# Optimization experiments

Measured on AMD Instinct MI355X. Metric: run time of the kernel, lower is better.

Reference implementation:

```python
import jax, jax.numpy as jnp
import numpy as np


def setup_inputs() -> dict:
    key = jax.random.key(0)
    ks = jax.random.split(key, 6)
    B, L, D, E = 4, 2048, 1024, 4
    H = 4 * D
    x = jax.random.normal(ks[0], (B, L, D), dtype=jnp.float32)
    # router: Linear(D, 2D) -> GELU -> Linear(2D, E); kaiming-ish init
    rW1 = jax.random.normal(ks[1], (D, 2 * D), dtype=jnp.float32) * (2.0 / D) ** 0.5
    rb1 = jnp.zeros((2 * D,), dtype=jnp.float32)
    rW2 = jax.random.normal(ks[2], (2 * D, E), dtype=jnp.float32) * (2.0 / (2 * D)) ** 0.5
    rb2 = jnp.zeros((E,), dtype=jnp.float32)
    # experts: Linear(D, 4D) -> GELU -> Linear(4D, D), stacked over E
    We1 = jax.random.normal(ks[3], (E, D, H), dtype=jnp.float32) * (2.0 / D) ** 0.5
    be1 = jnp.zeros((E, H), dtype=jnp.float32)
    We2 = jax.random.normal(ks[4], (E, H, D), dtype=jnp.float32) * (2.0 / H) ** 0.5
    be2 = jnp.zeros((E, D), dtype=jnp.float32)
    return {"x": x, "rW1": rW1, "rb1": rb1, "rW2": rW2, "rb2": rb2,
            "We1": We1, "be1": be1, "We2": We2, "be2": be2}


def reference(x, rW1, rb1, rW2, rb2, We1, be1, We2, be2):
    E = We1.shape[0]
    top_k = min(2, E)
    # router (dropouts are identity in eval mode)
    rh = jax.nn.gelu(x @ rW1 + rb1, approximate=False)          # [B,L,2D]
    router_logits = rh @ rW2 + rb2                               # [B,L,E]
    router_probs = jax.nn.softmax(router_logits, axis=-1)
    expert_weights, expert_indices = jax.lax.top_k(router_probs, top_k)  # [B,L,k]
    one_hot = jax.nn.one_hot(expert_indices, E, dtype=x.dtype)   # [B,L,k,E]
    token_mask = one_hot.sum(axis=2)                             # [B,L,E] 1 if expert selected
    combine_w = (one_hot * expert_weights[..., None]).sum(axis=2)  # [B,L,E] gate weight per expert
    out = jnp.zeros_like(x)
    for e in range(E):  # fixed small expert count; dense per-expert MLP over all tokens (as original)
        xi = x * token_mask[..., e:e + 1]
        h = jax.nn.gelu(xi @ We1[e] + be1[e], approximate=False)  # [B,L,4D]
        yo = h @ We2[e] + be2[e]                                  # [B,L,D]
        out = out + yo * combine_w[..., e:e + 1]
    return out
```

## Files before the change

### kernel.cpp

```cpp
#include <hip/hip_runtime.h>
#include <math.h>


typedef short bf16x8 __attribute__((ext_vector_type(8)));
typedef float f32x4 __attribute__((ext_vector_type(4)));
typedef unsigned short u16;

__device__ __forceinline__ u16 f2bf(float f) {
  unsigned u = __float_as_uint(f);
  u += 0x7FFFu + ((u >> 16) & 1u);
  return (u16)(u >> 16);
}
__device__ __forceinline__ float bf2f(u16 s) {
  return __uint_as_float(((unsigned)s) << 16);
}
__device__ __forceinline__ float gelu_f(float x) {
  return 0.5f * x * (1.0f + erff(x * 0.70710678118654752f));
}
__device__ __forceinline__ float gelu_fast(float x) {
  float y = 1.5957691216057308f * (x + 0.044715f * x * x * x);
  float e = __expf(y);
  float t = 1.0f - 2.0f * __builtin_amdgcn_rcpf(e + 1.0f);
  return 0.5f * x * (1.0f + t);
}
__device__ __forceinline__ void gload_lds16(const void* g, void* l) {
  __builtin_amdgcn_global_load_lds(
      (const __attribute__((address_space(1))) void*)g,
      (__attribute__((address_space(3))) void*)l, 16, 0, 0);
}

__global__ __launch_bounds__(256) void convert_split_kernel(
    const float* __restrict__ in, u16* __restrict__ hi, u16* __restrict__ lo,
    int n4) {
  int i = blockIdx.x * blockDim.x + threadIdx.x;
  int stride = gridDim.x * blockDim.x;
  for (; i < n4; i += stride) {
    float4 v = ((const float4*)in)[i];
    float f[4] = {v.x, v.y, v.z, v.w};
    ushort4 h4, l4;
    u16* hp = (u16*)&h4;
    u16* lp = (u16*)&l4;
#pragma unroll
    for (int u = 0; u < 4; ++u) {
      u16 h = f2bf(f[u]);
      hp[u] = h;
      lp[u] = f2bf(f[u] - bf2f(h));
    }
    ((ushort4*)hi)[i] = h4;
    ((ushort4*)lo)[i] = l4;
  }
}

__global__ __launch_bounds__(256) void transpose_split_kernel(
    const float* __restrict__ in, u16* __restrict__ hi, u16* __restrict__ lo,
    int R, int C) {
  __shared__ float tile[32][33];
  const int c0 = blockIdx.x * 32, r0 = blockIdx.y * 32;
#pragma unroll
  for (int i = 0; i < 4; ++i) {
    int rr = threadIdx.y + i * 8;
    tile[rr][threadIdx.x] = in[(size_t)(r0 + rr) * C + c0 + threadIdx.x];
  }
  __syncthreads();
#pragma unroll
  for (int i = 0; i < 4; ++i) {
    int cc = threadIdx.y + i * 8;
    float v = tile[threadIdx.x][cc];
    u16 h = f2bf(v);
    size_t oidx = (size_t)(c0 + cc) * R + r0 + threadIdx.x;
    hi[oidx] = h;
    lo[oidx] = f2bf(v - bf2f(h));
  }
}

__global__ __launch_bounds__(256) void transpose_pair_kernel(
    const float* __restrict__ We1, const float* __restrict__ We2,
    u16* __restrict__ T1, u16* __restrict__ T2, size_t tstride, int e0) {
  __shared__ float tile[32][33];
  const int e = e0 + blockIdx.y;
  int b = blockIdx.x;
  const float* in;
  u16* out;
  int R, C, tx, ty;
  if (b < 4096) {
    in = We1 + (size_t)e * 1024 * 4096;
    out = T1 + (size_t)blockIdx.y * tstride;
    R = 1024; C = 4096; tx = b & 127; ty = b >> 7;
  } else {
    b -= 4096;
    in = We2 + (size_t)e * 1024 * 4096;
    out = T2 + (size_t)blockIdx.y * tstride;
    R = 4096; C = 1024; tx = b & 31; ty = b >> 5;
  }
  const int c0 = tx * 32, r0 = ty * 32;
#pragma unroll
  for (int i = 0; i < 4; ++i) {
    int rr = threadIdx.y + i * 8;
    tile[rr][threadIdx.x] = in[(size_t)(r0 + rr) * C + c0 + threadIdx.x];
  }
  __syncthreads();
#pragma unroll
  for (int i = 0; i < 4; ++i) {
    int cc = threadIdx.y + i * 8;
    out[(size_t)(c0 + cc) * R + r0 + threadIdx.x] = f2bf(tile[threadIdx.x][cc]);
  }
}

__global__ __launch_bounds__(256) void gemm3_router_kernel(
    const u16* __restrict__ Ahi, const u16* __restrict__ Alo,
    const u16* __restrict__ Bhi, const u16* __restrict__ Blo, int K,
    const float* __restrict__ bias, const float* __restrict__ rW2,
    float* __restrict__ parts) {
  __shared__ alignas(16) u16 Sm[4 * 128 * 32];
  __shared__ float pls[2][128][4];
  const int tid = threadIdx.x;
  const int lane = tid & 63;
  const int w = tid >> 6;
  const int wr = w >> 1, wc = w & 1;

  const int flat = blockIdx.x + blockIdx.y * 16;
  const int swz = (flat & 7) * 128 + (flat >> 3);
  const int bxs = swz & 15;
  const int bys = swz >> 4;
  const int brow = bys * 128;
  const int bcol = bxs * 128;

  f32x4 acc[4][4] = {};
  char* S = (char*)Sm;
  const u16* srcs[4] = {Ahi + (size_t)brow * K, Alo + (size_t)brow * K,
                        Bhi + (size_t)bcol * K, Blo + (size_t)bcol * K};
  const int rA = lane & 15;
  const int kg2 = (lane >> 4) * 16;

  const int nk = K >> 5;
  for (int kt = 0; kt < nk; ++kt) {
    const int k0 = kt << 5;
    __syncthreads();
#pragma unroll
    for (int i = 0; i < 8; ++i) {
      int c = tid + 256 * i;
      int tile = c >> 9;
      int cc = c & 511;
      int row = cc >> 2;
      int kp = (cc & 3) << 3;
      gload_lds16(srcs[tile] + (size_t)row * K + (k0 + kp), S + c * 16);
    }
    __syncthreads();

    bf16x8 ah[4], al[4], bh[4], bl[4];
#pragma unroll
    for (int m = 0; m < 4; ++m) {
      int ro = (wr * 64 + m * 16 + rA) * 64 + kg2;
      ah[m] = *(const bf16x8*)(S + ro);
      al[m] = *(const bf16x8*)(S + 8192 + ro);
    }
#pragma unroll
    for (int n = 0; n < 4; ++n) {
      int ro = (wc * 64 + n * 16 + rA) * 64 + kg2;
      bh[n] = *(const bf16x8*)(S + 16384 + ro);
      bl[n] = *(const bf16x8*)(S + 24576 + ro);
    }
#pragma unroll
    for (int m = 0; m < 4; ++m)
#pragma unroll
      for (int n = 0; n < 4; ++n) {
        acc[m][n] = __builtin_amdgcn_mfma_f32_16x16x32_bf16(ah[m], bh[n], acc[m][n], 0, 0, 0);
        acc[m][n] = __builtin_amdgcn_mfma_f32_16x16x32_bf16(al[m], bh[n], acc[m][n], 0, 0, 0);
        acc[m][n] = __builtin_amdgcn_mfma_f32_16x16x32_bf16(ah[m], bl[n], acc[m][n], 0, 0, 0);
      }
  }

  const int cr = (lane >> 4) * 4;
  const int ccx = lane & 15;
  float4 w2v[4];
  float bv[4];
#pragma unroll
  for (int n = 0; n < 4; ++n) {
    const int gc = bcol + wc * 64 + n * 16 + ccx;
    w2v[n] = ((const float4*)rW2)[gc];
    bv[n] = bias[gc];
  }
#pragma unroll
  for (int m = 0; m < 4; ++m) {
    float pl[4][4];
#pragma unroll
    for (int r = 0; r < 4; ++r)
#pragma unroll
      for (int e = 0; e < 4; ++e) pl[r][e] = 0.f;
#pragma unroll
    for (int n = 0; n < 4; ++n)
#pragma unroll
      for (int r = 0; r < 4; ++r) {
        const float v = gelu_f(acc[m][n][r] + bv[n]);
        pl[r][0] += v * w2v[n].x;
        pl[r][1] += v * w2v[n].y;
        pl[r][2] += v * w2v[n].z;
        pl[r][3] += v * w2v[n].w;
      }
#pragma unroll
    for (int off = 8; off; off >>= 1)
#pragma unroll
      for (int r = 0; r < 4; ++r)
#pragma unroll
        for (int e = 0; e < 4; ++e) pl[r][e] += __shfl_xor(pl[r][e], off);
    if ((lane & 15) == 0) {
      const int row = wr * 64 + m * 16 + cr;
#pragma unroll
      for (int r = 0; r < 4; ++r)
#pragma unroll
        for (int e = 0; e < 4; ++e) pls[wc][row + r][e] = pl[r][e];
    }
  }
  __syncthreads();
  for (int i = tid; i < 512; i += 256) {
    const int row = i >> 2, e = i & 3;
    parts[((size_t)bxs * 8192 + brow + row) * 4 + e] =
        pls[0][row][e] + pls[1][row][e];
  }
}

__global__ __launch_bounds__(256) void topk_kernel(
    const float* __restrict__ parts, const float* __restrict__ rb2,
    float* __restrict__ combine, int* __restrict__ cnt, int* __restrict__ list,
    int2* __restrict__ tokslot, int T) {
  const int t = blockIdx.x * 256 + threadIdx.x;
  const int w = threadIdx.x >> 6, lane = threadIdx.x & 63;
  __shared__ int wpre[4][4];
  __shared__ int gbase[4];

  float lg[4] = {rb2[0], rb2[1], rb2[2], rb2[3]};
#pragma unroll
  for (int s = 0; s < 16; ++s) {
    float4 pv = ((const float4*)parts)[(size_t)s * 8192 + t];
    lg[0] += pv.x;
    lg[1] += pv.y;
    lg[2] += pv.z;
    lg[3] += pv.w;
  }
  float mx = fmaxf(fmaxf(lg[0], lg[1]), fmaxf(lg[2], lg[3]));
  float p[4], sum = 0.f;
#pragma unroll
  for (int e = 0; e < 4; ++e) {
    p[e] = expf(lg[e] - mx);
    sum += p[e];
  }
  float inv = 1.0f / sum;
  int i1 = 0;
#pragma unroll
  for (int e = 1; e < 4; ++e)
    if (lg[e] > lg[i1]) i1 = e;
  int i2 = -1;
#pragma unroll
  for (int e = 0; e < 4; ++e)
    if (e != i1 && (i2 < 0 || lg[e] > lg[i2])) i2 = e;
  float4 cw = {0.f, 0.f, 0.f, 0.f};
  ((float*)&cw)[i1] = p[i1] * inv;
  ((float*)&cw)[i2] = p[i2] * inv;
  ((float4*)combine)[t] = cw;

  unsigned long long m[4];
#pragma unroll
  for (int e = 0; e < 4; ++e) m[e] = __ballot(i1 == e || i2 == e);
  if (lane == 0) {
#pragma unroll
    for (int e = 0; e < 4; ++e) wpre[w][e] = (int)__popcll(m[e]);
  }
  __syncthreads();
  if (threadIdx.x < 4) {
    const int e = threadIdx.x;
    int tot = 0;
#pragma unroll
    for (int ww = 0; ww < 4; ++ww) {
      int c = wpre[ww][e];
      wpre[ww][e] = tot;
      tot += c;
    }
    gbase[e] = atomicAdd(&cnt[e], tot);
  }
  __syncthreads();
  const unsigned long long lt = (1ull << lane) - 1ull;
  int p1 = gbase[i1] + wpre[w][i1] + (int)__popcll(m[i1] & lt);
  list[i1 * 8192 + p1] = t;
  int p2 = gbase[i2] + wpre[w][i2] + (int)__popcll(m[i2] & lt);
  list[i2 * 8192 + p2] = t;
  tokslot[t] = make_int2(i1 * 8192 + p1, i2 * 8192 + p2);
}

__global__ void prefix_kernel(const int* __restrict__ cnt, int* __restrict__ pre) {
  if (threadIdx.x == 0) {
    int s = 0;
#pragma unroll
    for (int e = 0; e < 4; ++e) {
      pre[e] = s;
      s += cnt[e];
    }
  }
}

__global__ __launch_bounds__(512) void gemm_gather_kernel(
    const u16* __restrict__ A, const u16* __restrict__ WT, size_t wts,
    const int* __restrict__ list, const int* __restrict__ cnt_arr,
    const int* __restrict__ hbase_arr, int e0, const float* __restrict__ be1,
    u16* __restrict__ h) {
  const int K = 1024;
  const int e = e0 + blockIdx.z;
  const int cnt = cnt_arr[e];
  const int rb = blockIdx.y;
  if (rb * 128 >= cnt) return;
  const int hbase = hbase_arr[e];
  const int* lst = list + e * 8192;
  const u16* Bt = WT + (size_t)blockIdx.z * wts;
  const float* bias = be1 + e * 4096;

  __shared__ alignas(16) char lds[98304];
  const int tid = threadIdx.x;
  const int lane = tid & 63;
  const int w = tid >> 6;
  const int wr = w >> 2, wc = w & 3;
  const int bcol = blockIdx.x * 256;

  const int srow = tid >> 3;
  const int jx8 = (((tid & 7) ^ (srow & 7)) << 3);
  const u16* aS[2];
  const u16* bS[4];
#pragma unroll
  for (int i = 0; i < 2; ++i) {
    int g = rb * 128 + srow + 64 * i;
    int tok = lst[(g < cnt) ? g : rb * 128];
    aS[i] = A + (size_t)tok * K + jx8;
  }
#pragma unroll
  for (int i = 0; i < 4; ++i)
    bS[i] = Bt + (size_t)(bcol + srow + 64 * i) * K + jx8;
  const int dstb = tid * 16;

#define G_STAGE(kt, buf)                                                   \
  {                                                                        \
    const int kb_ = (kt) << 6;                                             \
    char* base_ = lds + (buf)*49152;                                       \
    _Pragma("unroll") for (int i = 0; i < 2; ++i)                          \
        gload_lds16(aS[i] + kb_, base_ + i * 8192 + dstb);                 \
    _Pragma("unroll") for (int i = 0; i < 4; ++i)                          \
        gload_lds16(bS[i] + kb_, base_ + 16384 + i * 8192 + dstb);         \
  }

  f32x4 acc[4][4] = {};
  const int rA = lane & 15;
  const int ksl = lane >> 4;
  const int rx7 = rA & 7;

  const int nk = K >> 6;
  int cur = 0;
  G_STAGE(0, 0);
  for (int kt = 0; kt < nk; ++kt) {
    if (kt + 1 < nk) {
      G_STAGE(kt + 1, cur ^ 1);
      asm volatile("s_waitcnt vmcnt(6)" ::: "memory");
    } else {
      asm volatile("s_waitcnt vmcnt(0)" ::: "memory");
    }
    __builtin_amdgcn_s_barrier();
    const char* Ab_ = lds + cur * 49152;
    const char* Bb_ = Ab_ + 16384;
#pragma unroll
    for (int s = 0; s < 2; ++s) {
      bf16x8 a[4], b[4];
      const int sl = (((s * 4 + ksl) ^ rx7) << 4);
#pragma unroll
      for (int m = 0; m < 4; ++m)
        a[m] = *(const bf16x8*)(Ab_ + (wr * 64 + m * 16 + rA) * 128 + sl);
#pragma unroll
      for (int n = 0; n < 4; ++n)
        b[n] = *(const bf16x8*)(Bb_ + (wc * 64 + n * 16 + rA) * 128 + sl);
#pragma unroll
      for (int m = 0; m < 4; ++m)
#pragma unroll
        for (int n = 0; n < 4; ++n)
          acc[m][n] =
              __builtin_amdgcn_mfma_f32_16x16x32_bf16(a[m], b[n], acc[m][n], 0, 0, 0);
    }
    __builtin_amdgcn_s_barrier();
    cur ^= 1;
  }
#undef G_STAGE

  const int cr = (lane >> 4) * 4;
  const int ccx = lane & 15;
#pragma unroll
  for (int m = 0; m < 4; ++m)
#pragma unroll
    for (int n = 0; n < 4; ++n) {
      const int gc = bcol + wc * 64 + n * 16 + ccx;
      const float bv = bias[gc];
#pragma unroll
      for (int r = 0; r < 4; ++r) {
        const int gl = rb * 128 + wr * 64 + m * 16 + cr + r;
        if (gl < cnt)
          h[(size_t)(hbase + gl) * 4096 + gc] = f2bf(gelu_fast(acc[m][n][r] + bv));
      }
    }
}

__global__ __launch_bounds__(512) void gemm_scatter_y_kernel(
    const u16* __restrict__ h, const int* __restrict__ hbase_arr,
    const u16* __restrict__ WT, size_t wts, const int* __restrict__ cnt_arr,
    int e0, const float* __restrict__ be2, u16* __restrict__ yout) {
  const int K = 4096;
  const int e = e0 + blockIdx.z;
  const int cnt = cnt_arr[e];
  const int rb = blockIdx.y;
  if (rb * 128 >= cnt) return;
  const int hbase = hbase_arr[e];
  const u16* Bt = WT + (size_t)blockIdx.z * wts;
  const float* bias = be2 + e * 1024;

  __shared__ alignas(16) char lds[98304];
  const int tid = threadIdx.x;
  const int lane = tid & 63;
  const int w = tid >> 6;
  const int wr = w >> 2, wc = w & 3;
  const int bcol = blockIdx.x * 256;

  const int srow = tid >> 3;
  const int jx8 = (((tid & 7) ^ (srow & 7)) << 3);
  const u16* aS[2];
  const u16* bS[4];
#pragma unroll
  for (int i = 0; i < 2; ++i)
    aS[i] = h + (size_t)(hbase + rb * 128 + srow + 64 * i) * K + jx8;
#pragma unroll
  for (int i = 0; i < 4; ++i)
    bS[i] = Bt + (size_t)(bcol + srow + 64 * i) * K + jx8;
  const int dstb = tid * 16;

#define S_STAGE(kt, buf)                                                   \
  {                                                                        \
    const int kb_ = (kt) << 6;                                             \
    char* base_ = lds + (buf)*49152;                                       \
    _Pragma("unroll") for (int i = 0; i < 2; ++i)                          \
        gload_lds16(aS[i] + kb_, base_ + i * 8192 + dstb);                 \
    _Pragma("unroll") for (int i = 0; i < 4; ++i)                          \
        gload_lds16(bS[i] + kb_, base_ + 16384 + i * 8192 + dstb);         \
  }

  f32x4 acc[4][4] = {};
  const int rA = lane & 15;
  const int ksl = lane >> 4;
  const int rx7 = rA & 7;

  const int nk = K >> 6;
  int cur = 0;
  S_STAGE(0, 0);
  for (int kt = 0; kt < nk; ++kt) {
    if (kt + 1 < nk) {
      S_STAGE(kt + 1, cur ^ 1);
      asm volatile("s_waitcnt vmcnt(6)" ::: "memory");
    } else {
      asm volatile("s_waitcnt vmcnt(0)" ::: "memory");
    }
    __builtin_amdgcn_s_barrier();
    const char* Ab_ = lds + cur * 49152;
    const char* Bb_ = Ab_ + 16384;
#pragma unroll
    for (int s = 0; s < 2; ++s) {
      bf16x8 a[4], b[4];
      const int sl = (((s * 4 + ksl) ^ rx7) << 4);
#pragma unroll
      for (int m = 0; m < 4; ++m)
        a[m] = *(const bf16x8*)(Ab_ + (wr * 64 + m * 16 + rA) * 128 + sl);
#pragma unroll
      for (int n = 0; n < 4; ++n)
        b[n] = *(const bf16x8*)(Bb_ + (wc * 64 + n * 16 + rA) * 128 + sl);
#pragma unroll
      for (int m = 0; m < 4; ++m)
#pragma unroll
        for (int n = 0; n < 4; ++n)
          acc[m][n] =
              __builtin_amdgcn_mfma_f32_16x16x32_bf16(a[m], b[n], acc[m][n], 0, 0, 0);
    }
    __builtin_amdgcn_s_barrier();
    cur ^= 1;
  }
#undef S_STAGE

  const int cr = (lane >> 4) * 4;
  const int ccx = lane & 15;
#pragma unroll
  for (int m = 0; m < 4; ++m)
#pragma unroll
    for (int r = 0; r < 4; ++r) {
      const int gl = rb * 128 + wr * 64 + m * 16 + cr + r;
      if (gl >= cnt) continue;
      u16* yrow = yout + (size_t)(hbase + gl) * 1024;
#pragma unroll
      for (int n = 0; n < 4; ++n) {
        const int gc = bcol + wc * 64 + n * 16 + ccx;
        yrow[gc] = f2bf(acc[m][n][r] + bias[gc]);
      }
    }
}

__global__ __launch_bounds__(256) void combine_kernel(
    const u16* __restrict__ yout, const int2* __restrict__ tokslot,
    const int* __restrict__ prefix, const float* __restrict__ gates,
    float* __restrict__ out) {
  const int w = threadIdx.x >> 6, lane = threadIdx.x & 63;
  const int t = blockIdx.x * 4 + w;
  const int2 s = tokslot[t];
  const int e1 = s.x >> 13, p1 = s.x & 8191;
  const int e2 = s.y >> 13, p2 = s.y & 8191;
  const int r1 = prefix[e1] + p1;
  const int r2 = prefix[e2] + p2;
  const float g1 = gates[(size_t)t * 4 + e1];
  const float g2 = gates[(size_t)t * 4 + e2];
  const ushort4* y1 = (const ushort4*)(yout + (size_t)r1 * 1024);
  const ushort4* y2 = (const ushort4*)(yout + (size_t)r2 * 1024);
  float4* o = (float4*)(out + (size_t)t * 1024);
#pragma unroll
  for (int j = 0; j < 4; ++j) {
    const int c = lane + j * 64;
    ushort4 a = y1[c], b = y2[c];
    float4 r;
    r.x = g1 * bf2f(a.x) + g2 * bf2f(b.x);
    r.y = g1 * bf2f(a.y) + g2 * bf2f(b.y);
    r.z = g1 * bf2f(a.z) + g2 * bf2f(b.z);
    r.w = g1 * bf2f(a.w) + g2 * bf2f(b.w);
    o[c] = r;
  }
}

__global__ __launch_bounds__(512) void gemm_scatter_kernel(
    const u16* __restrict__ h, const int* __restrict__ hbase_arr,
    const u16* __restrict__ WT, size_t wts, const int* __restrict__ list,
    const int* __restrict__ cnt_arr, int e0, const float* __restrict__ be2,
    const float* __restrict__ combine, float* __restrict__ out) {
  const int K = 4096;
  const int zslot = blockIdx.z >> 1;
  const int kz = blockIdx.z & 1;
  const int e = e0 + zslot;
  const int cnt = cnt_arr[e];
  const int rb = blockIdx.y;
  if (rb * 128 >= cnt) return;
  const int hbase = hbase_arr[e];
  const int* lst = list + e * 8192;
  const u16* Bt = WT + (size_t)zslot * wts;
  const float* bias = be2 + e * 1024;
  const int koff = kz * 2048;

  __shared__ alignas(16) u16 As[128 * 64];
  __shared__ alignas(16) u16 Bs[256 * 64];
  const int tid = threadIdx.x;
  const int lane = tid & 63;
  const int w = tid >> 6;
  const int wr = w >> 2, wc = w & 3;
  const int bcol = blockIdx.x * 256;

  const int srow = tid >> 3;
  const int jx8 = (((tid & 7) ^ (srow & 7)) << 3);
  const u16* aS[2];
  const u16* bS[4];
#pragma unroll
  for (int i = 0; i < 2; ++i)
    aS[i] = h + (size_t)(hbase + rb * 128 + srow + 64 * i) * K + koff + jx8;
#pragma unroll
  for (int i = 0; i < 4; ++i)
    bS[i] = Bt + (size_t)(bcol + srow + 64 * i) * K + koff + jx8;
  char* AsB = (char*)As;
  char* BsB = (char*)Bs;
  const int dstb = tid * 16;

  f32x4 acc[4][4] = {};
  const int rA = lane & 15;
  const int ksl = lane >> 4;
  const int rx7 = rA & 7;

  const int nk = 2048 >> 6;
  for (int kt = 0; kt < nk; ++kt) {
    const int kb = kt << 6;
    __syncthreads();
#pragma unroll
    for (int i = 0; i < 2; ++i)
      gload_lds16(aS[i] + kb, AsB + i * 8192 + dstb);
#pragma unroll
    for (int i = 0; i < 4; ++i)
      gload_lds16(bS[i] + kb, BsB + i * 8192 + dstb);
    __syncthreads();
#pragma unroll
    for (int s = 0; s < 2; ++s) {
      bf16x8 a[4], b[4];
      const int sl = (((s * 4 + ksl) ^ rx7) << 4);
#pragma unroll
      for (int m = 0; m < 4; ++m)
        a[m] = *(const bf16x8*)(AsB + (wr * 64 + m * 16 + rA) * 128 + sl);
#pragma unroll
      for (int n = 0; n < 4; ++n)
        b[n] = *(const bf16x8*)(BsB + (wc * 64 + n * 16 + rA) * 128 + sl);
#pragma unroll
      for (int m = 0; m < 4; ++m)
#pragma unroll
        for (int n = 0; n < 4; ++n)
          acc[m][n] =
              __builtin_amdgcn_mfma_f32_16x16x32_bf16(a[m], b[n], acc[m][n], 0, 0, 0);
    }
  }

  const int cr = (lane >> 4) * 4;
  const int ccx = lane & 15;
  const bool addb = (kz == 0);
#pragma unroll
  for (int m = 0; m < 4; ++m)
#pragma unroll
    for (int r = 0; r < 4; ++r) {
      const int gl = rb * 128 + wr * 64 + m * 16 + cr + r;
      if (gl >= cnt) continue;
      const int tok = lst[gl];
      const float gcoef = combine[(size_t)tok * 4 + e];
      float* orow = out + (size_t)tok * 1024;
#pragma unroll
      for (int n = 0; n < 4; ++n) {
        const int gc = bcol + wc * 64 + n * 16 + ccx;
        float v = acc[m][n][r];
        if (addb) v += bias[gc];
        atomicAdd(&orow[gc], gcoef * v);
      }
    }
}

extern "C" void kernel_launch(void* const* d_in, const int* in_sizes, int n_in,
                              void* d_out, int out_size, void* d_ws,
                              size_t ws_size, hipStream_t stream) {
  const float* x = (const float*)d_in[0];
  const float* rW1 = (const float*)d_in[1];
  const float* rb1 = (const float*)d_in[2];
  const float* rW2 = (const float*)d_in[3];
  const float* rb2 = (const float*)d_in[4];
  const float* We1 = (const float*)d_in[5];
  const float* be1 = (const float*)d_in[6];
  const float* We2 = (const float*)d_in[7];
  const float* be2 = (const float*)d_in[8];
  float* out = (float*)d_out;

  const int T = 8192, D = 1024, D2 = 2048, H = 4096, E = 4;
  const size_t WTS = (size_t)H * D;

  char* ws = (char*)d_ws;
  size_t off = 0;
  auto alloc = [&](size_t bytes) {
    char* p = ws + off;
    off = (off + bytes + 255) & ~(size_t)255;
    return p;
  };
  u16* x_hi = (u16*)alloc((size_t)T * D * 2);
  float* combine = (float*)alloc((size_t)T * 4 * 4);
  int* cnt = (int*)alloc(256);
  int* prefix = cnt + 4;
  int* list = (int*)alloc((size_t)4 * 8192 * 4);
  int2* tokslot = (int2*)alloc((size_t)T * 8);
  const size_t common_off = off;

  bool merged;
  u16 *We1T, *We2T, *h, *x_lo, *rW1T_hi, *rW1T_lo, *yout;
  float* parts;
  {
    size_t o = common_off;
    auto a2 = [&](size_t bytes) {
      char* p = ws + o;
      o = (o + bytes + 255) & ~(size_t)255;
      return p;
    };
    u16* w1 = (u16*)a2((size_t)4 * WTS * 2);
    u16* w2 = (u16*)a2((size_t)4 * WTS * 2);
    char* hreg = a2((size_t)16384 * H * 2 + (2u << 20));
    merged = (o <= ws_size);
    if (merged) {
      We1T = w1;
      We2T = w2;
      h = (u16*)hreg;
      yout = w1;
      x_lo = (u16*)hreg;
      rW1T_hi = (u16*)(hreg + (16u << 20));
      rW1T_lo = (u16*)(hreg + (20u << 20));
      parts = (float*)(hreg + (24u << 20));
    }
  }
  if (!merged) {
    off = common_off;
    We1T = (u16*)alloc(WTS * 2);
    We2T = (u16*)alloc(WTS * 2);
    x_lo = (u16*)alloc((size_t)T * D * 2);
    rW1T_hi = (u16*)alloc((size_t)D2 * D * 2);
    rW1T_lo = (u16*)alloc((size_t)D2 * D * 2);
    parts = (float*)alloc((size_t)16 * T * 4 * 4);
    h = (u16*)alloc((size_t)T * H * 2);
    yout = nullptr;
  }

  hipMemsetAsync(cnt, 0, 32, stream);
  if (!merged) hipMemsetAsync(out, 0, (size_t)T * D * 4, stream);

  dim3 tb(32, 8);

  convert_split_kernel<<<2048, 256, 0, stream>>>(x, x_hi, x_lo, T * D / 4);
  transpose_split_kernel<<<dim3(D2 / 32, D / 32), tb, 0, stream>>>(
      rW1, rW1T_hi, rW1T_lo, D, D2);
  gemm3_router_kernel<<<dim3(16, 64), 256, 0, stream>>>(
      x_hi, x_lo, rW1T_hi, rW1T_lo, D, rb1, rW2, parts);
  topk_kernel<<<T / 256, 256, 0, stream>>>(parts, rb2, combine, cnt, list,
                                           tokslot, T);

  if (merged) {
    prefix_kernel<<<1, 64, 0, stream>>>(cnt, prefix);
    transpose_pair_kernel<<<dim3(8192, 4), tb, 0, stream>>>(
        We1, We2, We1T, We2T, WTS, 0);
    gemm_gather_kernel<<<dim3(16, 64, 4), 512, 0, stream>>>(
        x_hi, We1T, WTS, list, cnt, prefix, 0, be1, h);
    gemm_scatter_y_kernel<<<dim3(4, 64, 4), 512, 0, stream>>>(
        h, prefix, We2T, WTS, cnt, 0, be2, yout);
    combine_kernel<<<T / 4, 256, 0, stream>>>(yout, tokslot, prefix, combine,
                                              out);
  } else {
    for (int e = 0; e < E; ++e) {
      transpose_pair_kernel<<<dim3(8192, 1), tb, 0, stream>>>(
          We1, We2, We1T, We2T, 0, e);
      gemm_gather_kernel<<<dim3(16, 64, 1), 512, 0, stream>>>(
          x_hi, We1T, 0, list, cnt, prefix , e, be1, h);
      gemm_scatter_kernel<<<dim3(4, 64, 2), 512, 0, stream>>>(
          h, prefix , We2T, 0, list, cnt, e, be2, combine, out);
    }
  }
}
```

Measured before the change: 644.5 us.

## Replace double-buffered LDS staging with single buffer in gather GEMM

The gathered expert up-projection GEMM drops its two-stage LDS ping-pong, in which the next K-tile was prefetched while the current one was computed. It now uses a single 48KB A/B tile buffer, loaded and consumed between two __syncthreads per K-step. This halves LDS use per block, which may let more blocks share a CU and hide latency through occupancy instead. In exchange, load and MFMA no longer overlap within a block, and each iteration adds a full barrier round trip.

```diff
diff --git a/kernel.cpp b/kernel.cpp
--- a/kernel.cpp
+++ b/kernel.cpp
@@ -312,7 +312,8 @@
   const u16* Bt = WT + (size_t)blockIdx.z * wts;
   const float* bias = be1 + e * 4096;
 
-  __shared__ alignas(16) char lds[98304];
+  __shared__ alignas(16) u16 As[128 * 64];
+  __shared__ alignas(16) u16 Bs[256 * 64];
   const int tid = threadIdx.x;
   const int lane = tid & 63;
   const int w = tid >> 6;
@@ -332,17 +333,9 @@
 #pragma unroll
   for (int i = 0; i < 4; ++i)
     bS[i] = Bt + (size_t)(bcol + srow + 64 * i) * K + jx8;
+  char* AsB = (char*)As;
+  char* BsB = (char*)Bs;
   const int dstb = tid * 16;
-
-#define G_STAGE(kt, buf)                                                   \
-  {                                                                        \
-    const int kb_ = (kt) << 6;                                             \
-    char* base_ = lds + (buf)*49152;                                       \
-    _Pragma("unroll") for (int i = 0; i < 2; ++i)                          \
-        gload_lds16(aS[i] + kb_, base_ + i * 8192 + dstb);                 \
-    _Pragma("unroll") for (int i = 0; i < 4; ++i)                          \
-        gload_lds16(bS[i] + kb_, base_ + 16384 + i * 8192 + dstb);         \
-  }
 
   f32x4 acc[4][4] = {};
   const int rA = lane & 15;
@@ -350,28 +343,26 @@
   const int rx7 = rA & 7;
 
   const int nk = K >> 6;
-  int cur = 0;
-  G_STAGE(0, 0);
   for (int kt = 0; kt < nk; ++kt) {
-    if (kt + 1 < nk) {
-      G_STAGE(kt + 1, cur ^ 1);
-      asm volatile("s_waitcnt vmcnt(6)" ::: "memory");
-    } else {
-      asm volatile("s_waitcnt vmcnt(0)" ::: "memory");
-    }
-    __builtin_amdgcn_s_barrier();
-    const char* Ab_ = lds + cur * 49152;
-    const char* Bb_ = Ab_ + 16384;
+    const int kb = kt << 6;
+    __syncthreads();
+#pragma unroll
+    for (int i = 0; i < 2; ++i)
+      gload_lds16(aS[i] + kb, AsB + i * 8192 + dstb);
+#pragma unroll
+    for (int i = 0; i < 4; ++i)
+      gload_lds16(bS[i] + kb, BsB + i * 8192 + dstb);
+    __syncthreads();
 #pragma unroll
     for (int s = 0; s < 2; ++s) {
       bf16x8 a[4], b[4];
       const int sl = (((s * 4 + ksl) ^ rx7) << 4);
 #pragma unroll
       for (int m = 0; m < 4; ++m)
-        a[m] = *(const bf16x8*)(Ab_ + (wr * 64 + m * 16 + rA) * 128 + sl);
+        a[m] = *(const bf16x8*)(AsB + (wr * 64 + m * 16 + rA) * 128 + sl);
 #pragma unroll
       for (int n = 0; n < 4; ++n)
-        b[n] = *(const bf16x8*)(Bb_ + (wc * 64 + n * 16 + rA) * 128 + sl);
+        b[n] = *(const bf16x8*)(BsB + (wc * 64 + n * 16 + rA) * 128 + sl);
 #pragma unroll
       for (int m = 0; m < 4; ++m)
 #pragma unroll
@@ -379,10 +370,7 @@
           acc[m][n] =
               __builtin_amdgcn_mfma_f32_16x16x32_bf16(a[m], b[n], acc[m][n], 0, 0, 0);
     }
-    __builtin_amdgcn_s_barrier();
-    cur ^= 1;
-  }
-#undef G_STAGE
+  }
 
   const int cr = (lane >> 4) * 4;
   const int ccx = lane & 15;
```

New measurement: 586.0 us. -9.1%, faster.
